# Kernel optimization log

Hardware: AMD Instinct MI355X
Metric: run time of the kernel (lower is better)

Reference implementation:

```python
import jax, jax.numpy as jnp
import numpy as np

D = 512  # input_size
H = 512  # hidden_size
N = 64   # batch
T = 512  # timesteps


def setup_inputs() -> dict:
    key = jax.random.key(0)
    k1, k2, k3, k4 = jax.random.split(key, 4)
    x = jax.random.normal(k1, (N, T, D), dtype=jnp.float32)
    h0 = jax.random.normal(k2, (N, H), dtype=jnp.float32)
    Wx = jax.random.normal(k3, (D, H), dtype=jnp.float32) / np.sqrt(D)
    Wh = jax.random.normal(k4, (H, H), dtype=jnp.float32) / np.sqrt(H)
    b = jnp.zeros((H,), dtype=jnp.float32)
    return {"x": x, "h0": h0, "Wx": Wx, "Wh": Wh, "b": b}


def reference(x, h0, Wx, Wh, b):
    # Precompute input projections for all timesteps in one big GEMM:
    # same math as per-step x_t @ Wx inside the loop.
    xWx = jnp.einsum('ntd,dh->nth', x, Wx) + b  # (N, T, H)

    def step(prev_h, xwx_t):
        next_h = jnp.tanh(prev_h @ Wh + xwx_t)  # (N, H)
        return next_h, next_h

    # scan over time: xWx transposed to (T, N, H)
    _, hs = jax.lax.scan(step, h0, jnp.swapaxes(xWx, 0, 1))
    return jnp.swapaxes(hs, 0, 1)  # (N, T, H)
```

## Files before the change

kernel.cpp:

```cpp
#include <hip/hip_runtime.h>
#include <hip/hip_bf16.h>

#define NB 64
#define TT 512
#define HH 512
#define DD 512

typedef __attribute__((ext_vector_type(8))) __bf16 bf16x8;
typedef __attribute__((ext_vector_type(4))) float f32x4;

__device__ __forceinline__ unsigned short f2bf_rn(float f) {
    union { float f; unsigned u; } v; v.f = f;
    unsigned r = v.u + 0x7FFFu + ((v.u >> 16) & 1u);
    return (unsigned short)(r >> 16);
}
__device__ __forceinline__ float bf2f(unsigned short s) {
    union { unsigned u; float f; } v; v.u = ((unsigned)s) << 16;
    return v.f;
}

__global__ __launch_bounds__(256) void wt_kernel(const float* __restrict__ Wx,
                                                 unsigned short* __restrict__ Wt) {
    const int bk = blockIdx.x >> 3, bn = blockIdx.x & 7;
    const int k0 = bk * 64, n0 = bn * 64;
    __shared__ float tile[64][65];
    const int t = threadIdx.x;
    const int kr = t >> 2, seg = t & 3;
    const float4* src = (const float4*)&Wx[(k0 + kr) * HH + n0 + seg * 16];
    float4 a = src[0], b = src[1], c = src[2], d = src[3];
    float vv[16];
    *(float4*)&vv[0] = a; *(float4*)&vv[4] = b; *(float4*)&vv[8] = c; *(float4*)&vv[12] = d;
#pragma unroll
    for (int q = 0; q < 16; ++q) tile[kr][seg * 16 + q] = vv[q];
    __syncthreads();
    const int nr = t >> 2;
    unsigned hu[8], lu[8];
#pragma unroll
    for (int i = 0; i < 8; ++i) {
        float f0 = tile[seg * 16 + 2 * i + 0][nr];
        float f1 = tile[seg * 16 + 2 * i + 1][nr];
        unsigned short h0 = f2bf_rn(f0); unsigned short l0 = f2bf_rn(f0 - bf2f(h0));
        unsigned short h1 = f2bf_rn(f1); unsigned short l1 = f2bf_rn(f1 - bf2f(h1));
        hu[i] = (unsigned)h0 | ((unsigned)h1 << 16);
        lu[i] = (unsigned)l0 | ((unsigned)l1 << 16);
    }
    unsigned short* dh = &Wt[(n0 + nr) * 1024 + k0 + seg * 16];
    unsigned short* dl = dh + 512;
    ((uint4*)dh)[0] = make_uint4(hu[0], hu[1], hu[2], hu[3]);
    ((uint4*)dh)[1] = make_uint4(hu[4], hu[5], hu[6], hu[7]);
    ((uint4*)dl)[0] = make_uint4(lu[0], lu[1], lu[2], lu[3]);
    ((uint4*)dl)[1] = make_uint4(lu[4], lu[5], lu[6], lu[7]);
}

#define LDA 72
__global__ __launch_bounds__(256) void proj_kernel(const float* __restrict__ x,
                                                   const unsigned short* __restrict__ Wt,
                                                   const float* __restrict__ bias,
                                                   float* __restrict__ out) {
    __shared__ __align__(16) unsigned short a_hi[64 * LDA];
    __shared__ __align__(16) unsigned short a_lo[64 * LDA];
    __shared__ __align__(16) unsigned short b_hi[64 * LDA];
    __shared__ __align__(16) unsigned short b_lo[64 * LDA];

    const int bx = blockIdx.x;
    const int i0 = (bx >> 3) * 64;
    const int n0 = (bx & 7) * 64;
    const int t = threadIdx.x;
    const int row = t >> 2, seg = t & 3;
    const int lane = t & 63, wid = t >> 6;
    const int wm = (wid >> 1) * 32, wn = (wid & 1) * 32;
    const int fr = lane & 15;

    f32x4 acc00 = {0.f, 0.f, 0.f, 0.f}, acc01 = acc00, acc10 = acc00, acc11 = acc00;

    for (int kc = 0; kc < 8; ++kc) {
        __syncthreads();
        {
            const float4* src = (const float4*)&x[(i0 + row) * DD + kc * 64 + seg * 16];
            float4 a = src[0], b = src[1], c = src[2], d = src[3];
            float vv[16];
            *(float4*)&vv[0] = a; *(float4*)&vv[4] = b; *(float4*)&vv[8] = c; *(float4*)&vv[12] = d;
            unsigned hu[8], lu[8];
#pragma unroll
            for (int i = 0; i < 8; ++i) {
                unsigned short h0 = f2bf_rn(vv[2 * i]); unsigned short l0 = f2bf_rn(vv[2 * i] - bf2f(h0));
                unsigned short h1 = f2bf_rn(vv[2 * i + 1]); unsigned short l1 = f2bf_rn(vv[2 * i + 1] - bf2f(h1));
                hu[i] = (unsigned)h0 | ((unsigned)h1 << 16);
                lu[i] = (unsigned)l0 | ((unsigned)l1 << 16);
            }
            uint4* dh = (uint4*)&a_hi[row * LDA + seg * 16];
            uint4* dl = (uint4*)&a_lo[row * LDA + seg * 16];
            dh[0] = make_uint4(hu[0], hu[1], hu[2], hu[3]);
            dh[1] = make_uint4(hu[4], hu[5], hu[6], hu[7]);
            dl[0] = make_uint4(lu[0], lu[1], lu[2], lu[3]);
            dl[1] = make_uint4(lu[4], lu[5], lu[6], lu[7]);
        }
        {
            const uint4* sh = (const uint4*)&Wt[(n0 + row) * 1024 + kc * 64 + seg * 16];
            const uint4* sl = (const uint4*)&Wt[(n0 + row) * 1024 + 512 + kc * 64 + seg * 16];
            uint4 h0v = sh[0], h1v = sh[1], l0v = sl[0], l1v = sl[1];
            uint4* dh = (uint4*)&b_hi[row * LDA + seg * 16];
            uint4* dl = (uint4*)&b_lo[row * LDA + seg * 16];
            dh[0] = h0v; dh[1] = h1v; dl[0] = l0v; dl[1] = l1v;
        }
        __syncthreads();
#pragma unroll
        for (int s = 0; s < 2; ++s) {
            const int ko = s * 32 + (lane >> 4) * 8;
            bf16x8 ah0 = *(const bf16x8*)&a_hi[(wm + fr) * LDA + ko];
            bf16x8 ah1 = *(const bf16x8*)&a_hi[(wm + 16 + fr) * LDA + ko];
            bf16x8 al0 = *(const bf16x8*)&a_lo[(wm + fr) * LDA + ko];
            bf16x8 al1 = *(const bf16x8*)&a_lo[(wm + 16 + fr) * LDA + ko];
            bf16x8 bh0 = *(const bf16x8*)&b_hi[(wn + fr) * LDA + ko];
            bf16x8 bh1 = *(const bf16x8*)&b_hi[(wn + 16 + fr) * LDA + ko];
            bf16x8 bl0 = *(const bf16x8*)&b_lo[(wn + fr) * LDA + ko];
            bf16x8 bl1 = *(const bf16x8*)&b_lo[(wn + 16 + fr) * LDA + ko];
            acc00 = __builtin_amdgcn_mfma_f32_16x16x32_bf16(ah0, bh0, acc00, 0, 0, 0);
            acc00 = __builtin_amdgcn_mfma_f32_16x16x32_bf16(ah0, bl0, acc00, 0, 0, 0);
            acc00 = __builtin_amdgcn_mfma_f32_16x16x32_bf16(al0, bh0, acc00, 0, 0, 0);
            acc01 = __builtin_amdgcn_mfma_f32_16x16x32_bf16(ah0, bh1, acc01, 0, 0, 0);
            acc01 = __builtin_amdgcn_mfma_f32_16x16x32_bf16(ah0, bl1, acc01, 0, 0, 0);
            acc01 = __builtin_amdgcn_mfma_f32_16x16x32_bf16(al0, bh1, acc01, 0, 0, 0);
            acc10 = __builtin_amdgcn_mfma_f32_16x16x32_bf16(ah1, bh0, acc10, 0, 0, 0);
            acc10 = __builtin_amdgcn_mfma_f32_16x16x32_bf16(ah1, bl0, acc10, 0, 0, 0);
            acc10 = __builtin_amdgcn_mfma_f32_16x16x32_bf16(al1, bh0, acc10, 0, 0, 0);
            acc11 = __builtin_amdgcn_mfma_f32_16x16x32_bf16(ah1, bh1, acc11, 0, 0, 0);
            acc11 = __builtin_amdgcn_mfma_f32_16x16x32_bf16(ah1, bl1, acc11, 0, 0, 0);
            acc11 = __builtin_amdgcn_mfma_f32_16x16x32_bf16(al1, bh1, acc11, 0, 0, 0);
        }
    }
    const float bc0 = bias[n0 + wn + fr];
    const float bc1 = bias[n0 + wn + 16 + fr];
#pragma unroll
    for (int r = 0; r < 4; ++r) {
        int rw0 = i0 + wm + (lane >> 4) * 4 + r;
        int rw1 = rw0 + 16;
        out[rw0 * HH + n0 + wn + fr]      = acc00[r] + bc0;
        out[rw0 * HH + n0 + wn + 16 + fr] = acc01[r] + bc1;
        out[rw1 * HH + n0 + wn + fr]      = acc10[r] + bc0;
        out[rw1 * HH + n0 + wn + 16 + fr] = acc11[r] + bc1;
    }
}

__global__ __launch_bounds__(512, 2) void rec_kernel(const float* __restrict__ h0,
                                                     const float* __restrict__ Wh,
                                                     float* __restrict__ out,
                                                     unsigned long long* __restrict__ pbuf) {
    const int b = blockIdx.x;
    const int g = b & 63;
    const int s = b >> 6;
    const int j = threadIdx.x;
    const int sj = j >> 7;
    const bool owner = (sj == s);
    const int jl = j & 127;
    const int idx = s - (s > sj ? 1 : 0);

    float w[128];
#pragma unroll
    for (int r = 0; r < 128; ++r) w[r] = Wh[(s * 128 + r) * HH + j];

    __shared__ float hsl[2][128];
    if (j < 128) hsl[0][j] = h0[g * HH + s * 128 + j];

    float xw = owner ? out[(g * TT + 0) * HH + j] : 0.f;
    __syncthreads();

#pragma unroll 1
    for (int t = 0; t < TT; ++t) {
        const int slot = t & 1;
        const unsigned tg = (unsigned)(t + 1);

        float p0 = 0.f, p1 = 0.f, p2 = 0.f, p3 = 0.f;
        const float4* h4 = (const float4*)&hsl[t & 1][0];
#pragma unroll
        for (int r4 = 0; r4 < 32; ++r4) {
            float4 hv = h4[r4];
            p0 = fmaf(w[4 * r4 + 0], hv.x, p0);
            p1 = fmaf(w[4 * r4 + 1], hv.y, p1);
            p2 = fmaf(w[4 * r4 + 2], hv.z, p2);
            p3 = fmaf(w[4 * r4 + 3], hv.w, p3);
        }
        float part = (p0 + p1) + (p2 + p3);

        if (!owner) {
            unsigned long long pv = ((unsigned long long)tg << 32) |
                                    (unsigned long long)__float_as_uint(part);
            __hip_atomic_store(&pbuf[(((unsigned)slot * NB + g) * 3 + idx) * HH + j], pv,
                               __ATOMIC_RELAXED, __HIP_MEMORY_SCOPE_AGENT);
        } else {
            float xwn = (t + 1 < TT) ? out[(g * TT + t + 1) * HH + j] : 0.f;
            const unsigned long long* a0 = &pbuf[(((unsigned)slot * NB + g) * 3 + 0) * HH + j];
            const unsigned long long* a1 = a0 + HH;
            const unsigned long long* a2 = a1 + HH;
            unsigned long long v0, v1, v2;
            do {
                v0 = __hip_atomic_load(a0, __ATOMIC_RELAXED, __HIP_MEMORY_SCOPE_AGENT);
                v1 = __hip_atomic_load(a1, __ATOMIC_RELAXED, __HIP_MEMORY_SCOPE_AGENT);
                v2 = __hip_atomic_load(a2, __ATOMIC_RELAXED, __HIP_MEMORY_SCOPE_AGENT);
            } while ((unsigned)(v0 >> 32) != tg || (unsigned)(v1 >> 32) != tg ||
                     (unsigned)(v2 >> 32) != tg);
            float v = part + __uint_as_float((unsigned)v0) + __uint_as_float((unsigned)v1) +
                      __uint_as_float((unsigned)v2) + xw;
            float hn = 1.f - 2.f / (__expf(2.f * v) + 1.f);
            out[(g * TT + t) * HH + j] = hn;
            hsl[(t + 1) & 1][jl] = hn;
            xw = xwn;
        }
        __syncthreads();
    }
}

extern "C" void kernel_launch(void* const* d_in, const int* in_sizes, int n_in,
                              void* d_out, int out_size, void* d_ws, size_t ws_size,
                              hipStream_t stream) {
    (void)in_sizes; (void)n_in; (void)out_size; (void)ws_size;
    const float* x  = (const float*)d_in[0];
    const float* h0 = (const float*)d_in[1];
    const float* Wx = (const float*)d_in[2];
    const float* Wh = (const float*)d_in[3];
    const float* bv = (const float*)d_in[4];
    float* out = (float*)d_out;

    const size_t PBUF_BYTES = 2ull * NB * 3 * HH * sizeof(unsigned long long);
    unsigned long long* pbuf = (unsigned long long*)d_ws;
    unsigned short* Wt = (unsigned short*)((char*)d_ws + PBUF_BYTES);

    hipMemsetAsync(pbuf, 0, PBUF_BYTES, stream);

    wt_kernel<<<64, 256, 0, stream>>>(Wx, Wt);

    proj_kernel<<<(32768 / 64) * (HH / 64), 256, 0, stream>>>(x, Wt, bv, out);

    rec_kernel<<<NB * 4, 512, 0, stream>>>(h0, Wh, out, pbuf);
}
```

Measured before the change: 898.8 us.

## Split recurrent dot product across k-groups with shared-memory reduction

Each thread now computes partial dot products for four output columns over a 32-row slice of the hidden chunk, instead of one column over all 128 rows. The four k-group partials are then combined through a shared-memory buffer before the cross-block exchange. This shortens the serial FMA chain per timestep and lets each thread read only a quarter of the hidden-state vector from LDS. In exchange it adds an extra __syncthreads and an LDS round-trip on every step of the latency-bound recurrence.

```diff
diff --git a/kernel.cpp b/kernel.cpp
--- a/kernel.cpp
+++ b/kernel.cpp
@@ -149,20 +149,26 @@
     const int b = blockIdx.x;
     const int g = b & 63;
     const int s = b >> 6;
-    const int j = threadIdx.x;
-    const int sj = j >> 7;
-    const bool owner = (sj == s);
-    const int jl = j & 127;
-    const int idx = s - (s > sj ? 1 : 0);
-
-    float w[128];
-#pragma unroll
-    for (int r = 0; r < 128; ++r) w[r] = Wh[(s * 128 + r) * HH + j];
+    const int tid = threadIdx.x;
+    const int c = tid & 127;
+    const int kg = tid >> 7;
+    const int jf = c + 128 * kg;
+    const bool isOwner = (kg == s);
+    const int idx = s - (s > kg ? 1 : 0);
+
+    float w[4][32];
+#pragma unroll
+    for (int r = 0; r < 32; ++r) {
+        const float* row = &Wh[(s * 128 + kg * 32 + r) * HH + c];
+#pragma unroll
+        for (int cc = 0; cc < 4; ++cc) w[cc][r] = row[128 * cc];
+    }
 
     __shared__ float hsl[2][128];
-    if (j < 128) hsl[0][j] = h0[g * HH + s * 128 + j];
-
-    float xw = owner ? out[(g * TT + 0) * HH + j] : 0.f;
+    __shared__ float red4[4][512];
+    if (tid < 128) hsl[0][tid] = h0[g * HH + s * 128 + tid];
+
+    float xw = isOwner ? out[(g * TT + 0) * HH + jf] : 0.f;
     __syncthreads();
 
 #pragma unroll 1
@@ -170,26 +176,42 @@
         const int slot = t & 1;
         const unsigned tg = (unsigned)(t + 1);
 
+        const float4* h4 = (const float4*)&hsl[slot][kg * 32];
         float p0 = 0.f, p1 = 0.f, p2 = 0.f, p3 = 0.f;
-        const float4* h4 = (const float4*)&hsl[t & 1][0];
-#pragma unroll
-        for (int r4 = 0; r4 < 32; ++r4) {
+#pragma unroll
+        for (int r4 = 0; r4 < 8; ++r4) {
             float4 hv = h4[r4];
-            p0 = fmaf(w[4 * r4 + 0], hv.x, p0);
-            p1 = fmaf(w[4 * r4 + 1], hv.y, p1);
-            p2 = fmaf(w[4 * r4 + 2], hv.z, p2);
-            p3 = fmaf(w[4 * r4 + 3], hv.w, p3);
-        }
-        float part = (p0 + p1) + (p2 + p3);
-
-        if (!owner) {
+            p0 = fmaf(w[0][4 * r4 + 0], hv.x, p0);
+            p0 = fmaf(w[0][4 * r4 + 1], hv.y, p0);
+            p0 = fmaf(w[0][4 * r4 + 2], hv.z, p0);
+            p0 = fmaf(w[0][4 * r4 + 3], hv.w, p0);
+            p1 = fmaf(w[1][4 * r4 + 0], hv.x, p1);
+            p1 = fmaf(w[1][4 * r4 + 1], hv.y, p1);
+            p1 = fmaf(w[1][4 * r4 + 2], hv.z, p1);
+            p1 = fmaf(w[1][4 * r4 + 3], hv.w, p1);
+            p2 = fmaf(w[2][4 * r4 + 0], hv.x, p2);
+            p2 = fmaf(w[2][4 * r4 + 1], hv.y, p2);
+            p2 = fmaf(w[2][4 * r4 + 2], hv.z, p2);
+            p2 = fmaf(w[2][4 * r4 + 3], hv.w, p2);
+            p3 = fmaf(w[3][4 * r4 + 0], hv.x, p3);
+            p3 = fmaf(w[3][4 * r4 + 1], hv.y, p3);
+            p3 = fmaf(w[3][4 * r4 + 2], hv.z, p3);
+            p3 = fmaf(w[3][4 * r4 + 3], hv.w, p3);
+        }
+
+        *(float4*)&red4[kg][4 * c] = make_float4(p0, p1, p2, p3);
+        __syncthreads();
+        float mine = red4[0][4 * c + kg] + red4[1][4 * c + kg] +
+                     red4[2][4 * c + kg] + red4[3][4 * c + kg];
+
+        if (!isOwner) {
             unsigned long long pv = ((unsigned long long)tg << 32) |
-                                    (unsigned long long)__float_as_uint(part);
-            __hip_atomic_store(&pbuf[(((unsigned)slot * NB + g) * 3 + idx) * HH + j], pv,
+                                    (unsigned long long)__float_as_uint(mine);
+            __hip_atomic_store(&pbuf[(((unsigned)slot * NB + g) * 3 + idx) * HH + jf], pv,
                                __ATOMIC_RELAXED, __HIP_MEMORY_SCOPE_AGENT);
         } else {
-            float xwn = (t + 1 < TT) ? out[(g * TT + t + 1) * HH + j] : 0.f;
-            const unsigned long long* a0 = &pbuf[(((unsigned)slot * NB + g) * 3 + 0) * HH + j];
+            float xwn = (t + 1 < TT) ? out[(g * TT + t + 1) * HH + jf] : 0.f;
+            const unsigned long long* a0 = &pbuf[(((unsigned)slot * NB + g) * 3 + 0) * HH + jf];
             const unsigned long long* a1 = a0 + HH;
             const unsigned long long* a2 = a1 + HH;
             unsigned long long v0, v1, v2;
@@ -199,11 +221,11 @@
                 v2 = __hip_atomic_load(a2, __ATOMIC_RELAXED, __HIP_MEMORY_SCOPE_AGENT);
             } while ((unsigned)(v0 >> 32) != tg || (unsigned)(v1 >> 32) != tg ||
                      (unsigned)(v2 >> 32) != tg);
-            float v = part + __uint_as_float((unsigned)v0) + __uint_as_float((unsigned)v1) +
+            float v = mine + __uint_as_float((unsigned)v0) + __uint_as_float((unsigned)v1) +
                       __uint_as_float((unsigned)v2) + xw;
             float hn = 1.f - 2.f / (__expf(2.f * v) + 1.f);
-            out[(g * TT + t) * HH + j] = hn;
-            hsl[(t + 1) & 1][jl] = hn;
+            out[(g * TT + t) * HH + jf] = hn;
+            hsl[(t + 1) & 1][c] = hn;
             xw = xwn;
         }
         __syncthreads();
```

Result: faster. 842.7 us (-6.2%).
